# Performance work log

Measured on AMD Instinct MI355X. Metric: run time of the kernel, lower is better.

## Reference

```python
import jax, jax.numpy as jnp
import numpy as np

N = 8192       # nodes
E = 131072     # edges
R = 4          # relations
IN_EMBD = 64   # per-feature embedding dim -> node feat = 6*64 = 384
H1 = 256       # layer_embd
D = 128        # out_embd; layer2 outputs 2*D
VOCABS = [35, 10, 5, 7, 5, 5]


def setup_inputs() -> dict:
    key = jax.random.key(0)
    ks = jax.random.split(key, 20)
    inp = {}
    inp['x'] = jax.random.randint(ks[0], (N, 6), 0, 5)
    inp['edge_index'] = jax.random.randint(ks[1], (2, E), 0, N)
    inp['edge_type'] = jax.random.randint(ks[2], (E,), 0, R)
    for i, v in enumerate(VOCABS):
        inp[f'emb{i}'] = jax.random.normal(ks[3 + i], (v, IN_EMBD), jnp.float32) * 0.1
    inp['W1'] = jax.random.normal(ks[10], (R, 6 * IN_EMBD, H1), jnp.float32) * 0.05
    inp['root1'] = jax.random.normal(ks[11], (6 * IN_EMBD, H1), jnp.float32) * 0.05
    inp['b1'] = jnp.zeros((H1,), jnp.float32)
    inp['W2'] = jax.random.normal(ks[12], (R, H1, 2 * D), jnp.float32) * 0.05
    inp['root2'] = jax.random.normal(ks[13], (H1, 2 * D), jnp.float32) * 0.05
    inp['b2'] = jnp.zeros((2 * D,), jnp.float32)
    return inp


def _rgcn(h, W, root, b, src, dst, edge_type):
    # RGCNConv (PyG semantics): out_i = root h_i + b + sum_r mean_{j in N_r(i)} W_r h_j
    out = h @ root + b
    for r in range(R):
        hr = h @ W[r]                                   # [N, out]
        m = (edge_type == r).astype(h.dtype)            # [E]
        s = jax.ops.segment_sum(hr[src] * m[:, None], dst, num_segments=N)
        c = jax.ops.segment_sum(m, dst, num_segments=N)
        out = out + s / jnp.clip(c, 1.0)[:, None]
    return out


def reference(x, edge_index, edge_type, emb0, emb1, emb2, emb3, emb4, emb5,
              W1, root1, b1, W2, root2, b2):
    embs = [emb0, emb1, emb2, emb3, emb4, emb5]
    x_ = jnp.concatenate([embs[i][x[:, i]] for i in range(6)], axis=1)  # [N, 384]
    src, dst = edge_index[0], edge_index[1]
    h1 = jax.nn.sigmoid(_rgcn(x_, W1, root1, b1, src, dst, edge_type))
    h2 = jax.nn.sigmoid(_rgcn(h1, W2, root2, b2, src, dst, edge_type))
    mu, logvar = h2[:, :D], h2[:, D:]
    std = jnp.exp(0.5 * logvar)
    eps = jax.random.normal(jax.random.key(42), std.shape, std.dtype)
    Z = eps * std + mu                                   # reparametrize
    A_hat = jax.nn.sigmoid(Z @ Z.T)                      # [N, N]
    A = jnp.zeros((N, N), jnp.float32).at[src, dst].set(1.0)
    return A, A_hat, mu, logvar
```

## Files before the change

### kernel.cpp

```cpp
#include <hip/hip_runtime.h>
#include <hip/hip_bf16.h>
#include <cstdint>
#include <cstddef>

#define N_NODES 8192
#define NE      131072
#define NR      4
#define NC      1280
#define SLOTS   96

typedef __attribute__((ext_vector_type(8))) short bf16x8;
typedef __attribute__((ext_vector_type(4))) float f32x4;

__device__ __forceinline__ float sigmoidf_(float x) {
  return 1.0f / (1.0f + __expf(-x));
}

__device__ __forceinline__ ushort f2b(float v) {
  __hip_bfloat16 h = __float2bfloat16(v);
  return *(ushort*)&h;
}
__device__ __forceinline__ float b2f(ushort u) {
  __hip_bfloat16 h = *(__hip_bfloat16*)&u;
  return __bfloat162float(h);
}
__device__ __forceinline__ void split2(float v, ushort& hi, ushort& lo) {
  hi = f2b(v);
  lo = f2b(v - b2f(hi));
}

__global__ void k_embed(const int* __restrict__ xi,
                        const float* __restrict__ e0, const float* __restrict__ e1,
                        const float* __restrict__ e2, const float* __restrict__ e3,
                        const float* __restrict__ e4, const float* __restrict__ e5,
                        ushort* __restrict__ xhi) {
  int n = blockIdx.x;
  int c = threadIdx.x;
  int i = c >> 6, d = c & 63;
  const float* t;
  switch (i) {
    case 0: t = e0; break; case 1: t = e1; break; case 2: t = e2; break;
    case 3: t = e3; break; case 4: t = e4; break; default: t = e5; break;
  }
  float v = t[(size_t)xi[n * 6 + i] * 64 + d];
  xhi[(size_t)n * 384 + c] = f2b(v);
}

__global__ __launch_bounds__(256) void k_pack_all(
    const float* __restrict__ r1, const float* __restrict__ W1,
    const float* __restrict__ r2, const float* __restrict__ W2,
    ushort* __restrict__ B1t, ushort* __restrict__ B2thi, ushort* __restrict__ B2tlo) {
  __shared__ ushort sh[64][66];
  __shared__ ushort sl[64][66];
  int b = blockIdx.x;
  int layer, K, kt, nt, seg;
  const float *srcR, *srcW;
  if (b < 120) { layer = 1; K = 384; int t = b;       seg = t / 24; t %= 24; kt = t / 4; nt = t % 4; srcR = r1; srcW = W1; }
  else         { layer = 2; K = 256; int t = b - 120; seg = t / 16; t %= 16; kt = t / 4; nt = t % 4; srcR = r2; srcW = W2; }
  int k0 = kt * 64, n0 = nt * 64;
  int tid = threadIdx.x;
#pragma unroll
  for (int it = 0; it < 16; ++it) {
    int idx = it * 256 + tid;
    int kl = idx >> 6, nl = idx & 63;
    int kg = k0 + kl, c = n0 + nl;
    float v = (seg == 0) ? srcR[(size_t)kg * 256 + c]
                         : srcW[((size_t)(seg - 1) * K + kg) * 256 + c];
    ushort h, l; split2(v, h, l);
    sh[kl][nl] = h;
    sl[kl][nl] = l;
  }
  __syncthreads();
#pragma unroll
  for (int it = 0; it < 16; ++it) {
    int idx = it * 256 + tid;
    int nl = idx >> 6, kl = idx & 63;
    size_t o = (size_t)(seg * 256 + n0 + nl) * K + k0 + kl;
    if (layer == 1) {
      B1t[o] = sh[kl][nl];
    } else {
      B2thi[o] = sh[kl][nl];
      B2tlo[o] = sl[kl][nl];
    }
  }
}

__global__ void k_fill_scatter(const int* __restrict__ src, const int* __restrict__ dst,
                               const int* __restrict__ et,
                               int* __restrict__ cnt, int* __restrict__ slots,
                               float* __restrict__ A) {
  int e = blockIdx.x * 256 + threadIdx.x;
  if (e < NE) {
    int d = dst[e], s = src[e];
    int pos = atomicAdd(&cnt[d], 1);
    if (pos < SLOTS) slots[(size_t)d * SLOTS + pos] = (s << 2) | et[e];
    A[(size_t)s * N_NODES + d] = 1.0f;
  }
}

template<int SPLIT3, int ACT, int SYM, int OUT>
__global__ __launch_bounds__(256) void k_gemm2(
    const ushort* __restrict__ Ahi, const ushort* __restrict__ Alo,
    const ushort* __restrict__ Bhi, const ushort* __restrict__ Blo,
    void* __restrict__ Cv, int Nc, int K) {
  __shared__ ushort Bs[(SPLIT3 ? 2 : 1) * 128 * 128];
  ushort* BsH = Bs;
  ushort* BsL = Bs + 128 * 128;

  const int tid = threadIdx.x;
  const int w = tid >> 6, l = tid & 63;
  const int lrow = l & 15, lk8 = (l >> 4) * 8;

  int brow, bcol, p = 0, q = 0;
  if (SYM) {
    int b = blockIdx.x;
    q = (int)((sqrtf(8.f * (float)b + 1.f) - 1.f) * 0.5f);
    while ((q + 1) * (q + 2) / 2 <= b) ++q;
    while (q * (q + 1) / 2 > b) --q;
    p = b - q * (q + 1) / 2;
    brow = p * 128; bcol = q * 128;
  } else {
    brow = blockIdx.y * 128; bcol = blockIdx.x * 128;
  }

  f32x4 acc[2][8] = {};
  const size_t arow0 = (size_t)(brow + w * 32 + lrow) * K + lk8;
  const size_t arow1 = arow0 + (size_t)16 * K;

  for (int kc = 0; kc < K; kc += 128) {
    bf16x8 aH[4][2], aL[4][2];
#pragma unroll
    for (int kk = 0; kk < 4; ++kk) {
      aH[kk][0] = *(const bf16x8*)(Ahi + arow0 + kc + kk * 32);
      aH[kk][1] = *(const bf16x8*)(Ahi + arow1 + kc + kk * 32);
      if (SPLIT3) {
        aL[kk][0] = *(const bf16x8*)(Alo + arow0 + kc + kk * 32);
        aL[kk][1] = *(const bf16x8*)(Alo + arow1 + kc + kk * 32);
      }
    }
    if (kc) __syncthreads();
#pragma unroll
    for (int it = 0; it < 8; ++it) {
      int o = (it * 256 + tid) * 16;
      int row = o >> 8, sb = o & 255;
      int se = (sb ^ ((row & 7) << 4)) >> 1;
      size_t g = (size_t)(bcol + row) * K + kc + se;
      *(uint4*)((char*)BsH + o) = *(const uint4*)(Bhi + g);
      if (SPLIT3) *(uint4*)((char*)BsL + o) = *(const uint4*)(Blo + g);
    }
    __syncthreads();
#pragma unroll
    for (int kk = 0; kk < 4; ++kk) {
#pragma unroll
      for (int n = 0; n < 8; ++n) {
        int row_t = n * 16 + lrow;
        int addr = row_t * 256 + ((kk * 64 + (l >> 4) * 16) ^ ((row_t & 7) << 4));
        bf16x8 b_h = *(const bf16x8*)((const char*)BsH + addr);
        acc[0][n] = __builtin_amdgcn_mfma_f32_16x16x32_bf16(aH[kk][0], b_h, acc[0][n], 0, 0, 0);
        acc[1][n] = __builtin_amdgcn_mfma_f32_16x16x32_bf16(aH[kk][1], b_h, acc[1][n], 0, 0, 0);
        if (SPLIT3) {
          bf16x8 b_l = *(const bf16x8*)((const char*)BsL + addr);
          acc[0][n] = __builtin_amdgcn_mfma_f32_16x16x32_bf16(aL[kk][0], b_h, acc[0][n], 0, 0, 0);
          acc[1][n] = __builtin_amdgcn_mfma_f32_16x16x32_bf16(aL[kk][1], b_h, acc[1][n], 0, 0, 0);
          acc[0][n] = __builtin_amdgcn_mfma_f32_16x16x32_bf16(aH[kk][0], b_l, acc[0][n], 0, 0, 0);
          acc[1][n] = __builtin_amdgcn_mfma_f32_16x16x32_bf16(aH[kk][1], b_l, acc[1][n], 0, 0, 0);
        }
      }
    }
  }

  const int crow = (l >> 4) * 4, ccol = l & 15;
  float*  Cf = (float*)Cv;
  ushort* Cb = (ushort*)Cv;
  const int domirror = (SYM && p != q);
  if (SYM) { if (domirror) __syncthreads(); }
  float* T = (float*)Bs;
#pragma unroll
  for (int m = 0; m < 2; ++m)
#pragma unroll
    for (int n = 0; n < 8; ++n) {
      float v[4];
#pragma unroll
      for (int r = 0; r < 4; ++r) {
        float t = acc[m][n][r];
        v[r] = ACT ? sigmoidf_(t) : t;
      }
      int rloc = w * 32 + m * 16 + crow;
      int cloc = n * 16 + ccol;
#pragma unroll
      for (int r = 0; r < 4; ++r) {
        if (OUT) Cb[(size_t)(brow + rloc + r) * Nc + bcol + cloc] = f2b(v[r]);
        else     Cf[(size_t)(brow + rloc + r) * Nc + bcol + cloc] = v[r];
      }
      if (SYM && p != q) {
        int s = (cloc & 7) << 2;
#pragma unroll
        for (int r = 0; r < 4; ++r) T[cloc * 128 + ((rloc + r) ^ s)] = v[r];
      }
    }
  if (SYM && p != q) {
    __syncthreads();
#pragma unroll
    for (int it = 0; it < 16; ++it) {
      int idx = it * 256 + tid;
      int rw = idx >> 5;
      int c4 = (idx & 31) * 4;
      int s = (rw & 7) << 2;
      float4 val = *(const float4*)&T[rw * 128 + (c4 ^ s)];
      *(float4*)(Cf + (size_t)(bcol + rw) * Nc + brow + c4) = val;
    }
  }
}

__device__ __forceinline__ float bits_to_normal(unsigned bits) {
  float f = __uint_as_float((bits >> 9) | 0x3f800000u) - 1.0f;
  const float lo = -0.99999994f;
  float u = __fadd_rn(__fmul_rn(f, 2.0f), lo);
  u = fmaxf(lo, u);
  float w = -log1pf(-u * u);
  float p;
  if (w < 5.0f) {
    w = w - 2.5f;
    p = 2.81022636e-08f;
    p = fmaf(p, w, 3.43273939e-07f);
    p = fmaf(p, w, -3.5233877e-06f);
    p = fmaf(p, w, -4.39150654e-06f);
    p = fmaf(p, w, 0.00021858087f);
    p = fmaf(p, w, -0.00125372503f);
    p = fmaf(p, w, -0.00417768164f);
    p = fmaf(p, w, 0.246640727f);
    p = fmaf(p, w, 1.50140941f);
  } else {
    w = sqrtf(w) - 3.0f;
    p = -0.000200214257f;
    p = fmaf(p, w, 0.000100950558f);
    p = fmaf(p, w, 0.00134934322f);
    p = fmaf(p, w, -0.00367342844f);
    p = fmaf(p, w, 0.00573950773f);
    p = fmaf(p, w, -0.0076224613f);
    p = fmaf(p, w, 0.00943887047f);
    p = fmaf(p, w, 1.00167406f);
    p = fmaf(p, w, 2.83297682f);
  }
  return 1.41421356f * (p * u);
}

__device__ __forceinline__ unsigned threefry_bits(unsigned j) {
  const unsigned ks0 = 0u, ks1 = 42u, ks2 = 0x1BD11BDAu ^ 0u ^ 42u;
  unsigned x0 = 0u + ks0;
  unsigned x1 = j + ks1;
#define RND(r) { x0 += x1; x1 = (x1 << r) | (x1 >> (32 - r)); x1 ^= x0; }
  RND(13) RND(15) RND(26) RND(6)  x0 += ks1; x1 += ks2 + 1u;
  RND(17) RND(29) RND(16) RND(24) x0 += ks2; x1 += ks0 + 2u;
  RND(13) RND(15) RND(26) RND(6)  x0 += ks0; x1 += ks1 + 3u;
  RND(17) RND(29) RND(16) RND(24) x0 += ks1; x1 += ks2 + 4u;
  RND(13) RND(15) RND(26) RND(6)  x0 += ks2; x1 += ks0 + 5u;
#undef RND
  return x0 ^ x1;
}

__global__ __launch_bounds__(256) void k_combine1(
    const ushort* __restrict__ hall, const float* __restrict__ bias,
    const int* __restrict__ cnt, const int* __restrict__ slots,
    ushort* __restrict__ h_hi, ushort* __restrict__ h_lo) {
  __shared__ int sc[64];
  int n = blockIdx.x, c = threadIdx.x;
  int end = min(cnt[n], SLOTS);
  const int* sl = slots + (size_t)n * SLOTS;
  float a0 = 0.f, a1 = 0.f, a2 = 0.f, a3 = 0.f;
  int c0 = 0, c1 = 0, c2 = 0, c3 = 0;
  for (int base = 0; base < end; base += 64) {
    int mcnt = min(64, end - base);
    if (c < 64 && base + c < end) sc[c] = sl[base + c];
    __syncthreads();
    int i = 0;
    for (; i + 4 <= mcnt; i += 4) {
      int p0 = sc[i], p1 = sc[i + 1], p2 = sc[i + 2], p3 = sc[i + 3];
      float v0 = b2f(hall[(size_t)(p0 >> 2) * NC + 256 + (size_t)(p0 & 3) * 256 + c]);
      float v1 = b2f(hall[(size_t)(p1 >> 2) * NC + 256 + (size_t)(p1 & 3) * 256 + c]);
      float v2 = b2f(hall[(size_t)(p2 >> 2) * NC + 256 + (size_t)(p2 & 3) * 256 + c]);
      float v3 = b2f(hall[(size_t)(p3 >> 2) * NC + 256 + (size_t)(p3 & 3) * 256 + c]);
      int r;
      r = p0 & 3; if (r == 0) { a0 += v0; ++c0; } else if (r == 1) { a1 += v0; ++c1; }
                  else if (r == 2) { a2 += v0; ++c2; } else { a3 += v0; ++c3; }
      r = p1 & 3; if (r == 0) { a0 += v1; ++c0; } else if (r == 1) { a1 += v1; ++c1; }
                  else if (r == 2) { a2 += v1; ++c2; } else { a3 += v1; ++c3; }
      r = p2 & 3; if (r == 0) { a0 += v2; ++c0; } else if (r == 1) { a1 += v2; ++c1; }
                  else if (r == 2) { a2 += v2; ++c2; } else { a3 += v2; ++c3; }
      r = p3 & 3; if (r == 0) { a0 += v3; ++c0; } else if (r == 1) { a1 += v3; ++c1; }
                  else if (r == 2) { a2 += v3; ++c2; } else { a3 += v3; ++c3; }
    }
    for (; i < mcnt; ++i) {
      int pp = sc[i];
      int r = pp & 3;
      float v = b2f(hall[(size_t)(pp >> 2) * NC + 256 + (size_t)r * 256 + c]);
      if (r == 0) { a0 += v; ++c0; } else if (r == 1) { a1 += v; ++c1; }
      else if (r == 2) { a2 += v; ++c2; } else { a3 += v; ++c3; }
    }
    __syncthreads();
  }
  float v = b2f(hall[(size_t)n * NC + c]) + bias[c]
          + a0 / (float)max(c0, 1) + a1 / (float)max(c1, 1)
          + a2 / (float)max(c2, 1) + a3 / (float)max(c3, 1);
  float sg = sigmoidf_(v);
  ushort h, l; split2(sg, h, l);
  h_hi[(size_t)n * 256 + c] = h;
  h_lo[(size_t)n * 256 + c] = l;
}

__global__ __launch_bounds__(256) void k_combine2z(
    const float* __restrict__ hall, const float* __restrict__ bias,
    const int* __restrict__ cnt, const int* __restrict__ slots,
    float* __restrict__ muo, float* __restrict__ lvo,
    ushort* __restrict__ zhi, ushort* __restrict__ zlo) {
  __shared__ int sc[64];
  __shared__ float sv[256];
  int n = blockIdx.x, c = threadIdx.x;
  int end = min(cnt[n], SLOTS);
  const int* sl = slots + (size_t)n * SLOTS;
  float a0 = 0.f, a1 = 0.f, a2 = 0.f, a3 = 0.f;
  int c0 = 0, c1 = 0, c2 = 0, c3 = 0;
  for (int base = 0; base < end; base += 64) {
    int mcnt = min(64, end - base);
    if (c < 64 && base + c < end) sc[c] = sl[base + c];
    __syncthreads();
    int i = 0;
    for (; i + 4 <= mcnt; i += 4) {
      int p0 = sc[i], p1 = sc[i + 1], p2 = sc[i + 2], p3 = sc[i + 3];
      float v0 = hall[(size_t)(p0 >> 2) * NC + 256 + (size_t)(p0 & 3) * 256 + c];
      float v1 = hall[(size_t)(p1 >> 2) * NC + 256 + (size_t)(p1 & 3) * 256 + c];
      float v2 = hall[(size_t)(p2 >> 2) * NC + 256 + (size_t)(p2 & 3) * 256 + c];
      float v3 = hall[(size_t)(p3 >> 2) * NC + 256 + (size_t)(p3 & 3) * 256 + c];
      int r;
      r = p0 & 3; if (r == 0) { a0 += v0; ++c0; } else if (r == 1) { a1 += v0; ++c1; }
                  else if (r == 2) { a2 += v0; ++c2; } else { a3 += v0; ++c3; }
      r = p1 & 3; if (r == 0) { a0 += v1; ++c0; } else if (r == 1) { a1 += v1; ++c1; }
                  else if (r == 2) { a2 += v1; ++c2; } else { a3 += v1; ++c3; }
      r = p2 & 3; if (r == 0) { a0 += v2; ++c0; } else if (r == 1) { a1 += v2; ++c1; }
                  else if (r == 2) { a2 += v2; ++c2; } else { a3 += v2; ++c3; }
      r = p3 & 3; if (r == 0) { a0 += v3; ++c0; } else if (r == 1) { a1 += v3; ++c1; }
                  else if (r == 2) { a2 += v3; ++c2; } else { a3 += v3; ++c3; }
    }
    for (; i < mcnt; ++i) {
      int pp = sc[i];
      int r = pp & 3;
      float v = hall[(size_t)(pp >> 2) * NC + 256 + (size_t)r * 256 + c];
      if (r == 0) { a0 += v; ++c0; } else if (r == 1) { a1 += v; ++c1; }
      else if (r == 2) { a2 += v; ++c2; } else { a3 += v; ++c3; }
    }
    __syncthreads();
  }
  float v = hall[(size_t)n * NC + c] + bias[c]
          + a0 / (float)max(c0, 1) + a1 / (float)max(c1, 1)
          + a2 / (float)max(c2, 1) + a3 / (float)max(c3, 1);
  float sg = sigmoidf_(v);
  if (c < 128) muo[(size_t)n * 128 + c] = sg;
  else         lvo[(size_t)n * 128 + (c - 128)] = sg;
  sv[c] = sg;
  __syncthreads();
  if (c < 128) {
    unsigned j = (unsigned)n * 128u + (unsigned)c;
    float e = bits_to_normal(threefry_bits(j));
    float z = fmaf(e, __expf(0.5f * sv[c + 128]), sv[c]);
    ushort h, l; split2(z, h, l);
    zhi[j] = h; zlo[j] = l;
  }
}

__global__ void k_zerof4(float4* __restrict__ p, size_t n4) {
  size_t i = (size_t)blockIdx.x * blockDim.x + threadIdx.x;
  size_t stride = (size_t)gridDim.x * blockDim.x;
  float4 z = make_float4(0.f, 0.f, 0.f, 0.f);
  for (; i < n4; i += stride) p[i] = z;
}

extern "C" void kernel_launch(void* const* d_in, const int* in_sizes, int n_in,
                              void* d_out, int out_size, void* d_ws, size_t ws_size,
                              hipStream_t stream) {
  const int* x    = (const int*)d_in[0];
  const int* ei   = (const int*)d_in[1];
  const int* src  = ei;
  const int* dst  = ei + NE;
  const int* et   = (const int*)d_in[2];
  const float* e0 = (const float*)d_in[3];
  const float* e1 = (const float*)d_in[4];
  const float* e2 = (const float*)d_in[5];
  const float* e3 = (const float*)d_in[6];
  const float* e4 = (const float*)d_in[7];
  const float* e5 = (const float*)d_in[8];
  const float* W1 = (const float*)d_in[9];
  const float* r1 = (const float*)d_in[10];
  const float* b1 = (const float*)d_in[11];
  const float* W2 = (const float*)d_in[12];
  const float* r2 = (const float*)d_in[13];
  const float* b2 = (const float*)d_in[14];

  float* out  = (float*)d_out;
  float* A    = out;
  float* Ahat = out + (size_t)N_NODES * N_NODES;
  float* muo  = Ahat + (size_t)N_NODES * N_NODES;
  float* lvo  = muo + (size_t)N_NODES * 128;

  char* wp = (char*)d_ws;
  auto carve = [&](size_t bytes) { char* r = wp; wp += (bytes + 255) & ~(size_t)255; return r; };
  ushort* xhi   = (ushort*)carve((size_t)8192 * 384 * 2);
  ushort* B1t   = (ushort*)carve((size_t)NC * 384 * 2);
  ushort* B2thi = (ushort*)carve((size_t)NC * 256 * 2);
  ushort* B2tlo = (ushort*)carve((size_t)NC * 256 * 2);
  float*  hall  = (float*)carve((size_t)8192 * NC * 4);
  ushort* hallb = (ushort*)hall;
  ushort* h1hi  = (ushort*)carve((size_t)8192 * 256 * 2);
  ushort* h1lo  = (ushort*)carve((size_t)8192 * 256 * 2);
  ushort* zhi   = (ushort*)carve((size_t)8192 * 128 * 2);
  ushort* zlo   = (ushort*)carve((size_t)8192 * 128 * 2);
  int*    cnt   = (int*)carve((size_t)8192 * 4);
  int*    slots = (int*)carve((size_t)8192 * SLOTS * 4);

  k_zerof4<<<8192, 256, 0, stream>>>((float4*)A, (size_t)N_NODES * N_NODES / 4);
  hipMemsetAsync(cnt, 0, (size_t)8192 * 4, stream);
  k_fill_scatter<<<NE / 256, 256, 0, stream>>>(src, dst, et, cnt, slots, A);

  k_embed<<<8192, 384, 0, stream>>>(x, e0, e1, e2, e3, e4, e5, xhi);
  k_pack_all<<<200, 256, 0, stream>>>(r1, W1, r2, W2, B1t, B2thi, B2tlo);

  k_gemm2<0, 0, 0, 1><<<dim3(NC / 128, 64), 256, 0, stream>>>(
      xhi, nullptr, B1t, nullptr, hallb, NC, 384);
  k_combine1<<<8192, 256, 0, stream>>>(hallb, b1, cnt, slots, h1hi, h1lo);

  k_gemm2<1, 0, 0, 0><<<dim3(NC / 128, 64), 256, 0, stream>>>(
      h1hi, h1lo, B2thi, B2tlo, hall, NC, 256);
  k_combine2z<<<8192, 256, 0, stream>>>(hall, b2, cnt, slots, muo, lvo, zhi, zlo);

  k_gemm2<1, 1, 1, 0><<<dim3(64 * 65 / 2), 256, 0, stream>>>(
      zhi, zlo, zhi, zlo, Ahat, N_NODES, 128);
}
```

Baseline: 291.1 us.

## Build adjacency rows in LDS and fuse embedding gather into first GEMM

After: 295.2 us. About the same (+1.4%).

```diff
diff --git a/kernel.cpp b/kernel.cpp
--- a/kernel.cpp
+++ b/kernel.cpp
@@ -28,22 +28,11 @@
   hi = f2b(v);
   lo = f2b(v - b2f(hi));
 }
-
-__global__ void k_embed(const int* __restrict__ xi,
-                        const float* __restrict__ e0, const float* __restrict__ e1,
-                        const float* __restrict__ e2, const float* __restrict__ e3,
-                        const float* __restrict__ e4, const float* __restrict__ e5,
-                        ushort* __restrict__ xhi) {
-  int n = blockIdx.x;
-  int c = threadIdx.x;
-  int i = c >> 6, d = c & 63;
-  const float* t;
-  switch (i) {
-    case 0: t = e0; break; case 1: t = e1; break; case 2: t = e2; break;
-    case 3: t = e3; break; case 4: t = e4; break; default: t = e5; break;
-  }
-  float v = t[(size_t)xi[n * 6 + i] * 64 + d];
-  xhi[(size_t)n * 384 + c] = f2b(v);
+__device__ __forceinline__ bf16x8 pack8(float4 a, float4 b) {
+  bf16x8 r;
+  r[0] = (short)f2b(a.x); r[1] = (short)f2b(a.y); r[2] = (short)f2b(a.z); r[3] = (short)f2b(a.w);
+  r[4] = (short)f2b(b.x); r[5] = (short)f2b(b.y); r[6] = (short)f2b(b.z); r[7] = (short)f2b(b.w);
+  return r;
 }
 
 __global__ __launch_bounds__(256) void k_pack_all(
@@ -85,17 +74,112 @@
   }
 }
 
-__global__ void k_fill_scatter(const int* __restrict__ src, const int* __restrict__ dst,
-                               const int* __restrict__ et,
-                               int* __restrict__ cnt, int* __restrict__ slots,
-                               float* __restrict__ A) {
+__global__ void k_fill2(const int* __restrict__ src, const int* __restrict__ dst,
+                        const int* __restrict__ et,
+                        int* __restrict__ cnt, int* __restrict__ slots,
+                        int* __restrict__ cnt2, int* __restrict__ slots2) {
   int e = blockIdx.x * 256 + threadIdx.x;
   if (e < NE) {
     int d = dst[e], s = src[e];
     int pos = atomicAdd(&cnt[d], 1);
     if (pos < SLOTS) slots[(size_t)d * SLOTS + pos] = (s << 2) | et[e];
-    A[(size_t)s * N_NODES + d] = 1.0f;
-  }
+    int pos2 = atomicAdd(&cnt2[s], 1);
+    if (pos2 < SLOTS) slots2[(size_t)s * SLOTS + pos2] = d;
+  }
+}
+
+__global__ __launch_bounds__(256) void k_arow(const int* __restrict__ cnt2,
+                                              const int* __restrict__ slots2,
+                                              float* __restrict__ A) {
+  __shared__ float row[N_NODES];
+  int n = blockIdx.x, tid = threadIdx.x;
+  float4 z = make_float4(0.f, 0.f, 0.f, 0.f);
+#pragma unroll
+  for (int it = 0; it < 8; ++it)
+    *(float4*)&row[(it * 256 + tid) * 4] = z;
+  __syncthreads();
+  int m = min(cnt2[n], SLOTS);
+  if (tid < m) row[slots2[(size_t)n * SLOTS + tid]] = 1.0f;
+  __syncthreads();
+  float4* out4 = (float4*)(A + (size_t)n * N_NODES);
+#pragma unroll
+  for (int it = 0; it < 8; ++it) {
+    int i = it * 256 + tid;
+    out4[i] = *(const float4*)&row[i * 4];
+  }
+}
+
+__global__ __launch_bounds__(256) void k_gemm1e(
+    const int* __restrict__ x,
+    const float* __restrict__ e0, const float* __restrict__ e1,
+    const float* __restrict__ e2, const float* __restrict__ e3,
+    const float* __restrict__ e4, const float* __restrict__ e5,
+    const ushort* __restrict__ Bhi, ushort* __restrict__ Cb) {
+  constexpr int K = 384;
+  __shared__ ushort BsH[128 * 128];
+  const int tid = threadIdx.x;
+  const int w = tid >> 6, l = tid & 63;
+  const int lrow = l & 15, lk8 = (l >> 4) * 8;
+  const int brow = blockIdx.y * 128, bcol = blockIdx.x * 128;
+  const int r0 = brow + w * 32 + lrow, r1i = r0 + 16;
+
+  int idx0[6], idx1[6];
+#pragma unroll
+  for (int j = 0; j < 3; ++j) {
+    int2 a = *(const int2*)(x + (size_t)r0 * 6 + j * 2);
+    idx0[j * 2] = a.x; idx0[j * 2 + 1] = a.y;
+    int2 b = *(const int2*)(x + (size_t)r1i * 6 + j * 2);
+    idx1[j * 2] = b.x; idx1[j * 2 + 1] = b.y;
+  }
+  const float* tabs[6] = {e0, e1, e2, e3, e4, e5};
+
+  f32x4 acc[2][8] = {};
+#pragma unroll
+  for (int kc = 0; kc < K; kc += 128) {
+    bf16x8 aH[4][2];
+#pragma unroll
+    for (int kk = 0; kk < 4; ++kk) {
+      const int base = kc + kk * 32;
+      const int ti = base >> 6;
+      const int dd = (base & 63) + lk8;
+      const float* t0 = tabs[ti] + (size_t)idx0[ti] * 64 + dd;
+      const float* t1 = tabs[ti] + (size_t)idx1[ti] * 64 + dd;
+      aH[kk][0] = pack8(*(const float4*)t0, *(const float4*)(t0 + 4));
+      aH[kk][1] = pack8(*(const float4*)t1, *(const float4*)(t1 + 4));
+    }
+    if (kc) __syncthreads();
+#pragma unroll
+    for (int it = 0; it < 8; ++it) {
+      int o = (it * 256 + tid) * 16;
+      int row = o >> 8, sb = o & 255;
+      int se = (sb ^ ((row & 7) << 4)) >> 1;
+      size_t g = (size_t)(bcol + row) * K + kc + se;
+      *(uint4*)((char*)BsH + o) = *(const uint4*)(Bhi + g);
+    }
+    __syncthreads();
+#pragma unroll
+    for (int kk = 0; kk < 4; ++kk) {
+#pragma unroll
+      for (int n = 0; n < 8; ++n) {
+        int row_t = n * 16 + lrow;
+        int addr = row_t * 256 + ((kk * 64 + (l >> 4) * 16) ^ ((row_t & 7) << 4));
+        bf16x8 b_h = *(const bf16x8*)((const char*)BsH + addr);
+        acc[0][n] = __builtin_amdgcn_mfma_f32_16x16x32_bf16(aH[kk][0], b_h, acc[0][n], 0, 0, 0);
+        acc[1][n] = __builtin_amdgcn_mfma_f32_16x16x32_bf16(aH[kk][1], b_h, acc[1][n], 0, 0, 0);
+      }
+    }
+  }
+  const int crow = (l >> 4) * 4, ccol = l & 15;
+#pragma unroll
+  for (int m = 0; m < 2; ++m)
+#pragma unroll
+    for (int n = 0; n < 8; ++n) {
+      int rloc = w * 32 + m * 16 + crow;
+      int cloc = n * 16 + ccol;
+#pragma unroll
+      for (int r = 0; r < 4; ++r)
+        Cb[(size_t)(brow + rloc + r) * NC + bcol + cloc] = f2b(acc[m][n][r]);
+    }
 }
 
 template<int SPLIT3, int ACT, int SYM, int OUT>
@@ -367,13 +451,6 @@
   }
 }
 
-__global__ void k_zerof4(float4* __restrict__ p, size_t n4) {
-  size_t i = (size_t)blockIdx.x * blockDim.x + threadIdx.x;
-  size_t stride = (size_t)gridDim.x * blockDim.x;
-  float4 z = make_float4(0.f, 0.f, 0.f, 0.f);
-  for (; i < n4; i += stride) p[i] = z;
-}
-
 extern "C" void kernel_launch(void* const* d_in, const int* in_sizes, int n_in,
                               void* d_out, int out_size, void* d_ws, size_t ws_size,
                               hipStream_t stream) {
@@ -403,28 +480,29 @@
 
   char* wp = (char*)d_ws;
   auto carve = [&](size_t bytes) { char* r = wp; wp += (bytes + 255) & ~(size_t)255; return r; };
-  ushort* xhi   = (ushort*)carve((size_t)8192 * 384 * 2);
-  ushort* B1t   = (ushort*)carve((size_t)NC * 384 * 2);
-  ushort* B2thi = (ushort*)carve((size_t)NC * 256 * 2);
-  ushort* B2tlo = (ushort*)carve((size_t)NC * 256 * 2);
-  float*  hall  = (float*)carve((size_t)8192 * NC * 4);
-  ushort* hallb = (ushort*)hall;
-  ushort* h1hi  = (ushort*)carve((size_t)8192 * 256 * 2);
-  ushort* h1lo  = (ushort*)carve((size_t)8192 * 256 * 2);
-  ushort* zhi   = (ushort*)carve((size_t)8192 * 128 * 2);
-  ushort* zlo   = (ushort*)carve((size_t)8192 * 128 * 2);
-  int*    cnt   = (int*)carve((size_t)8192 * 4);
-  int*    slots = (int*)carve((size_t)8192 * SLOTS * 4);
-
-  k_zerof4<<<8192, 256, 0, stream>>>((float4*)A, (size_t)N_NODES * N_NODES / 4);
-  hipMemsetAsync(cnt, 0, (size_t)8192 * 4, stream);
-  k_fill_scatter<<<NE / 256, 256, 0, stream>>>(src, dst, et, cnt, slots, A);
-
-  k_embed<<<8192, 384, 0, stream>>>(x, e0, e1, e2, e3, e4, e5, xhi);
+  ushort* B1t    = (ushort*)carve((size_t)NC * 384 * 2);
+  ushort* B2thi  = (ushort*)carve((size_t)NC * 256 * 2);
+  ushort* B2tlo  = (ushort*)carve((size_t)NC * 256 * 2);
+  float*  hall   = (float*)carve((size_t)8192 * NC * 4);
+  ushort* hallb  = (ushort*)hall;
+  ushort* h1hi   = (ushort*)carve((size_t)8192 * 256 * 2);
+  ushort* h1lo   = (ushort*)carve((size_t)8192 * 256 * 2);
+  ushort* zhi    = (ushort*)carve((size_t)8192 * 128 * 2);
+  ushort* zlo    = (ushort*)carve((size_t)8192 * 128 * 2);
+  int*    cnt    = (int*)carve((size_t)8192 * 4);
+  int*    cnt2   = (int*)carve((size_t)8192 * 4);
+  int*    slots  = (int*)carve((size_t)8192 * SLOTS * 4);
+  int*    slots2 = (int*)carve((size_t)8192 * SLOTS * 4);
+
+  hipMemsetAsync(cnt, 0, (size_t)2 * 8192 * 4, stream);
+  k_fill2<<<NE / 256, 256, 0, stream>>>(src, dst, et, cnt, slots, cnt2, slots2);
+
+  k_arow<<<8192, 256, 0, stream>>>(cnt2, slots2, A);
+
   k_pack_all<<<200, 256, 0, stream>>>(r1, W1, r2, W2, B1t, B2thi, B2tlo);
 
-  k_gemm2<0, 0, 0, 1><<<dim3(NC / 128, 64), 256, 0, stream>>>(
-      xhi, nullptr, B1t, nullptr, hallb, NC, 384);
+  k_gemm1e<<<dim3(NC / 128, 64), 256, 0, stream>>>(
+      x, e0, e1, e2, e3, e4, e5, B1t, hallb);
   k_combine1<<<8192, 256, 0, stream>>>(hallb, b1, cnt, slots, h1hi, h1lo);
 
   k_gemm2<1, 0, 0, 0><<<dim3(NC / 128, 64), 256, 0, stream>>>(
```
